# Performance work log

Hardware: AMD Instinct MI355X
Metric: run time of the kernel (lower is better)

## Reference

```python
import jax, jax.numpy as jnp
import numpy as np

N_NODES = 20000
N_EDGES = 320000
D_IN = 256      # n_source_nodes (input feature dim)
HEADS = 4
HEAD_DIM = 64   # n_target_nodes // heads
D_OUT = HEADS * HEAD_DIM  # n_target_nodes = 256
EDGE_DIM = 1


def setup_inputs() -> dict:
    key = jax.random.key(0)
    ks = jax.random.split(key, 12)
    s = 0.05
    return {
        "x": jax.random.normal(ks[0], (N_NODES, D_IN), jnp.float32),
        "edge_index": jax.random.randint(ks[1], (2, N_EDGES), 0, N_NODES, jnp.int64),
        "edge_attr": jax.random.normal(ks[2], (N_EDGES, EDGE_DIM), jnp.float32),
        # TransformerConv params (weights stored [in, out]; PyG Linear defaults: q/k/v have bias, edge lin has no bias, skip lin has bias)
        "Wq": jax.random.normal(ks[3], (D_IN, D_OUT), jnp.float32) * s,
        "bq": jnp.zeros((D_OUT,), jnp.float32),
        "Wk": jax.random.normal(ks[4], (D_IN, D_OUT), jnp.float32) * s,
        "bk": jnp.zeros((D_OUT,), jnp.float32),
        "Wv": jax.random.normal(ks[5], (D_IN, D_OUT), jnp.float32) * s,
        "bv": jnp.zeros((D_OUT,), jnp.float32),
        "We": jax.random.normal(ks[6], (EDGE_DIM, D_OUT), jnp.float32) * s,
        "Wskip": jax.random.normal(ks[7], (D_IN, D_OUT), jnp.float32) * s,
        "bskip": jnp.zeros((D_OUT,), jnp.float32),
        # GraphNorm params
        "gn_weight": jnp.ones((D_OUT,), jnp.float32),
        "gn_bias": jnp.zeros((D_OUT,), jnp.float32),
        "gn_mean_scale": jnp.ones((D_OUT,), jnp.float32),
    }


def reference(x, edge_index, edge_attr, Wq, bq, Wk, bk, Wv, bv, We, Wskip, bskip, gn_weight, gn_bias, gn_mean_scale):
    N = x.shape[0]
    src, dst = edge_index[0], edge_index[1]  # message flows src -> dst (source_to_target)

    q = (x @ Wq + bq).reshape(N, HEADS, HEAD_DIM)
    k = (x @ Wk + bk).reshape(N, HEADS, HEAD_DIM)
    v = (x @ Wv + bv).reshape(N, HEADS, HEAD_DIM)
    e = (edge_attr @ We).reshape(-1, HEADS, HEAD_DIM)  # [E, H, C]

    k_j = k[src] + e                                   # [E, H, C]
    alpha = jnp.einsum('ehc,ehc->eh', q[dst], k_j) / jnp.sqrt(jnp.float32(HEAD_DIM))

    # segment softmax over edges sharing the same target node
    a_max = jax.ops.segment_max(alpha, dst, num_segments=N)[dst]
    a_exp = jnp.exp(alpha - a_max)
    a_sum = jax.ops.segment_sum(a_exp, dst, num_segments=N)[dst]
    att = a_exp / (a_sum + 1e-16)                      # [E, H]

    msg = (v[src] + e) * att[..., None]                # [E, H, C]
    out = jax.ops.segment_sum(msg, dst, num_segments=N).reshape(N, D_OUT)
    out = out + x @ Wskip + bskip                      # root/skip connection (beta=False)

    # GraphNorm (single graph): weight*(x - alpha*mean)/sqrt(var+eps) + bias
    mean = out.mean(axis=0)
    centered = out - gn_mean_scale * mean
    var = jnp.mean(centered * centered, axis=0)
    out = gn_weight * centered * jax.lax.rsqrt(var + 1e-5) + gn_bias

    out = jax.nn.relu(out)
    xt = out.T @ out                                   # [D_OUT, D_OUT]
    xt_min, xt_max = jnp.min(xt), jnp.max(xt)
    return (xt - xt_min) / (xt_max - xt_min + 1e-8)
```

## Files before the change

### kernel.cpp

```cpp
#include <hip/hip_runtime.h>
#include <math.h>

#define N_NODES 20000
#define N_EDGES 320000
#define SK 20480

typedef short short8 __attribute__((ext_vector_type(8)));
typedef float f32x4 __attribute__((ext_vector_type(4)));

static __device__ __forceinline__ unsigned short f2bf(float f) {
    unsigned int u = __float_as_uint(f);
    u = (u + 0x7FFF + ((u >> 16) & 1)) >> 16;
    return (unsigned short)u;
}
static __device__ __forceinline__ float b2f(unsigned short u) {
    return __uint_as_float((unsigned int)u << 16);
}
static __device__ __forceinline__ float blo(unsigned int u) {
    return __uint_as_float(u << 16);
}
static __device__ __forceinline__ float bhi(unsigned int u) {
    return __uint_as_float(u & 0xFFFF0000u);
}

__global__ __launch_bounds__(256) void conv_x_k(const float* __restrict__ x,
                                                unsigned short* __restrict__ xb)
{
    const int t8 = blockIdx.x * 256 + threadIdx.x;
    const size_t base = (size_t)t8 * 8;
    if (base >= (size_t)N_NODES * 256) return;
    const float4 f0 = *(const float4*)(x + base);
    const float4 f1 = *(const float4*)(x + base + 4);
    ushort4 u0, u1;
    u0.x = f2bf(f0.x); u0.y = f2bf(f0.y); u0.z = f2bf(f0.z); u0.w = f2bf(f0.w);
    u1.x = f2bf(f1.x); u1.y = f2bf(f1.y); u1.z = f2bf(f1.z); u1.w = f2bf(f1.w);
    *(ushort4*)(xb + base) = u0;
    *(ushort4*)(xb + base + 4) = u1;
}

__global__ __launch_bounds__(256) void conv_w_k(const float* __restrict__ Wq,
                                                const float* __restrict__ Wk,
                                                const float* __restrict__ Wv,
                                                const float* __restrict__ Wsk,
                                                const float* __restrict__ bq,
                                                const float* __restrict__ bk,
                                                const float* __restrict__ bv,
                                                const float* __restrict__ bsk,
                                                unsigned short* __restrict__ wT,
                                                float* __restrict__ bias_all)
{
    const int b = blockIdx.x;
    const int kk = threadIdx.x;
    const int wi = b >> 8, n = b & 255;
    const float* W = (wi == 0) ? Wq : (wi == 1) ? Wk : (wi == 2) ? Wv : Wsk;
    wT[(size_t)b * 256 + kk] = f2bf(W[(size_t)kk * 256 + n]);
    if (kk == 0) {
        const float* bb = (wi == 0) ? bq : (wi == 1) ? bk : (wi == 2) ? bv : bsk;
        bias_all[b] = bb[n];
    }
}

__global__ __launch_bounds__(512, 2) void gemm_qkvs(const unsigned short* __restrict__ xb,
                                                    const unsigned short* __restrict__ wT,
                                                    const float* __restrict__ bias_all,
                                                    float* __restrict__ qb,
                                                    unsigned short* __restrict__ kvb,
                                                    float* __restrict__ ob)
{
    __shared__ __align__(16) unsigned short As[(128 + 256) * 80];
    unsigned short* Bs = As + 128 * 80;
    float* stage = (float*)As;

    const int tid  = threadIdx.x;
    const int lane = tid & 63;
    const int w    = tid >> 6;
    const int wm = w >> 2, wn = w & 3;
    const int row0 = blockIdx.x * 128;
    const int wsel = blockIdx.y;
    const int colG = wsel * 256;
    const int ar = tid >> 2, ak = (tid & 3) * 16;
    const int br = tid >> 1, bk = (tid & 1) * 32;
    const int fr = lane & 15, fk = (lane >> 4) * 8, lg = lane >> 4;

    f32x4 acc[4][4] = {};

    for (int k0 = 0; k0 < 256; k0 += 64) {
        int gr = row0 + ar; gr = gr < N_NODES ? gr : N_NODES - 1;
        const unsigned short* ap = xb + (size_t)gr * 256 + k0 + ak;
        const uint4 a0 = *(const uint4*)ap;
        const uint4 a1 = *(const uint4*)(ap + 8);
        const unsigned short* bp = wT + (size_t)(colG + br) * 256 + k0 + bk;
        const uint4 b0 = *(const uint4*)bp;
        const uint4 b1 = *(const uint4*)(bp + 8);
        const uint4 b2 = *(const uint4*)(bp + 16);
        const uint4 b3 = *(const uint4*)(bp + 24);
        __syncthreads();
        *(uint4*)&As[ar * 80 + ak]     = a0;
        *(uint4*)&As[ar * 80 + ak + 8] = a1;
        unsigned short* bsp = &Bs[br * 80 + bk];
        *(uint4*)bsp        = b0;
        *(uint4*)(bsp + 8)  = b1;
        *(uint4*)(bsp + 16) = b2;
        *(uint4*)(bsp + 24) = b3;
        __syncthreads();
#pragma unroll
        for (int ks = 0; ks < 2; ++ks) {
            short8 af[4], bf[4];
#pragma unroll
            for (int m = 0; m < 4; ++m)
                af[m] = *(const short8*)&As[(wm * 64 + m * 16 + fr) * 80 + ks * 32 + fk];
#pragma unroll
            for (int n = 0; n < 4; ++n)
                bf[n] = *(const short8*)&Bs[(wn * 64 + n * 16 + fr) * 80 + ks * 32 + fk];
#pragma unroll
            for (int m = 0; m < 4; ++m)
#pragma unroll
                for (int n = 0; n < 4; ++n)
                    acc[m][n] = __builtin_amdgcn_mfma_f32_16x16x32_bf16(af[m], bf[n], acc[m][n], 0, 0, 0);
        }
    }
    __syncthreads();

    float badd[4];
#pragma unroll
    for (int n = 0; n < 4; ++n) badd[n] = bias_all[colG + wn * 64 + n * 16 + fr];

    float* st = stage + w * 1024;
#pragma unroll
    for (int m = 0; m < 4; ++m) {
#pragma unroll
        for (int n = 0; n < 4; ++n)
#pragma unroll
            for (int r = 0; r < 4; ++r)
                st[(lg * 4 + r) * 64 + n * 16 + fr] = acc[m][n][r] + badd[n];
#pragma unroll
        for (int it = 0; it < 4; ++it) {
            const int lrow = it * 4 + lg;
            const f32x4 c4 = *(const f32x4*)&st[lrow * 64 + fr * 4];
            const int grow = row0 + wm * 64 + m * 16 + lrow;
            if (grow < N_NODES) {
                if (wsel == 0) {
                    float4 o; o.x = c4[0]; o.y = c4[1]; o.z = c4[2]; o.w = c4[3];
                    *(float4*)(qb + (size_t)grow * 256 + wn * 64 + fr * 4) = o;
                } else if (wsel == 3) {
                    float4 o; o.x = c4[0]; o.y = c4[1]; o.z = c4[2]; o.w = c4[3];
                    *(float4*)(ob + (size_t)grow * 256 + wn * 64 + fr * 4) = o;
                } else {
                    ushort4 u;
                    u.x = f2bf(c4[0]); u.y = f2bf(c4[1]); u.z = f2bf(c4[2]); u.w = f2bf(c4[3]);
                    const size_t kvidx = (size_t)grow * 512 + (wn * 16 + fr) * 8 + (wsel == 1 ? 0 : 4);
                    *(ushort4*)(kvb + kvidx) = u;
                }
            }
        }
    }
}

__global__ void count_deg(const int* __restrict__ dst, int* __restrict__ deg)
{
    const int e = blockIdx.x * 256 + threadIdx.x;
    if (e < N_EDGES) atomicAdd(&deg[dst[e]], 1);
}

__global__ __launch_bounds__(1024) void scan_k(const int* __restrict__ deg,
                                               int* __restrict__ row_start)
{
    __shared__ int sdeg[20480];
    const int tid = threadIdx.x;
    const int lane = tid & 63, wid = tid >> 6;
    const int CH = 20;
#pragma unroll
    for (int i = 0; i < 20; ++i) {
        const int idx = i * 1024 + tid;
        sdeg[idx] = (idx < N_NODES) ? deg[idx] : 0;
    }
    __syncthreads();
    const int base = tid * CH;
    int local[CH];
    int s = 0;
#pragma unroll
    for (int i = 0; i < CH; ++i) {
        local[i] = s;
        s += sdeg[base + i];
    }
    int v = s;
#pragma unroll
    for (int off = 1; off < 64; off <<= 1) {
        const int t = __shfl_up(v, off);
        if (lane >= off) v += t;
    }
    __shared__ int wsum[16];
    if (lane == 63) wsum[wid] = v;
    __syncthreads();
    if (tid == 0) {
        int r = 0;
        for (int i = 0; i < 16; ++i) { const int t = wsum[i]; wsum[i] = r; r += t; }
    }
    __syncthreads();
    const int excl = v - s + wsum[wid];
#pragma unroll
    for (int i = 0; i < CH; ++i) {
        const int idx = base + i;
        if (idx < N_NODES) row_start[idx] = excl + local[i];
    }
    if (tid == 1023) row_start[N_NODES] = excl + s;
}

__global__ void fill_csr(const int* __restrict__ dst, const int* __restrict__ src,
                         const float* __restrict__ ea,
                         const int* __restrict__ row_start,
                         int* __restrict__ cursor, int2* __restrict__ ekv)
{
    const int e = blockIdx.x * 256 + threadIdx.x;
    if (e < N_EDGES) {
        const int d = dst[e];
        const int p = atomicAdd(&cursor[d], 1);
        int2 pk;
        pk.x = src[e];
        pk.y = __float_as_int(ea[e]);
        ekv[row_start[d] + p] = pk;
    }
}

static __device__ __forceinline__ void edge_step(const uint4 kv, const float a,
                                                 const float4 qf, const float4 we4,
                                                 float& ssum, float& ax, float& ay,
                                                 float& az, float& aw)
{
    const float k0 = blo(kv.x), k1 = bhi(kv.x), k2 = blo(kv.y), k3 = bhi(kv.y);
    const float v0 = blo(kv.z), v1 = bhi(kv.z), v2 = blo(kv.w), v3 = bhi(kv.w);
    float p = qf.x * (k0 + a * we4.x) + qf.y * (k1 + a * we4.y)
            + qf.z * (k2 + a * we4.z) + qf.w * (k3 + a * we4.w);
    p += __shfl_xor(p, 1); p += __shfl_xor(p, 2);
    p += __shfl_xor(p, 4); p += __shfl_xor(p, 8);
    const float wgt = __expf(p * 0.125f);
    ssum += wgt;
    ax += wgt * (v0 + a * we4.x);
    ay += wgt * (v1 + a * we4.y);
    az += wgt * (v2 + a * we4.z);
    aw += wgt * (v3 + a * we4.w);
}

__global__ __launch_bounds__(256) void attn_k(const float* __restrict__ q,
                                              const unsigned short* __restrict__ kvb,
                                              const float* __restrict__ We,
                                              const int* __restrict__ row_start,
                                              const int2* __restrict__ ekv,
                                              float* __restrict__ out)
{
    const int wid  = threadIdx.x >> 6;
    const int lane = threadIdx.x & 63;
    const int n = blockIdx.x * 4 + wid;
    if (n >= N_NODES) return;

    const float4 qf  = *(const float4*)(q + (size_t)n * 256 + lane * 4);
    const float4 we4 = *(const float4*)(We + lane * 4);
    const int rs = row_start[n], re = row_start[n + 1];
    const int lo8 = lane * 8;

    float ssum = 0.f;
    float ax = 0.f, ay = 0.f, az = 0.f, aw = 0.f;

    int s = rs;
    for (; s + 4 <= re; s += 4) {
        const int2 p0 = ekv[s],     p1 = ekv[s + 1];
        const int2 p2 = ekv[s + 2], p3 = ekv[s + 3];
        const int sn0 = ((unsigned)p0.x < N_NODES) ? p0.x : 0;
        const int sn1 = ((unsigned)p1.x < N_NODES) ? p1.x : 0;
        const int sn2 = ((unsigned)p2.x < N_NODES) ? p2.x : 0;
        const int sn3 = ((unsigned)p3.x < N_NODES) ? p3.x : 0;
        const uint4 kv0 = *(const uint4*)(kvb + (size_t)sn0 * 512 + lo8);
        const uint4 kv1 = *(const uint4*)(kvb + (size_t)sn1 * 512 + lo8);
        const uint4 kv2 = *(const uint4*)(kvb + (size_t)sn2 * 512 + lo8);
        const uint4 kv3 = *(const uint4*)(kvb + (size_t)sn3 * 512 + lo8);
        edge_step(kv0, __int_as_float(p0.y), qf, we4, ssum, ax, ay, az, aw);
        edge_step(kv1, __int_as_float(p1.y), qf, we4, ssum, ax, ay, az, aw);
        edge_step(kv2, __int_as_float(p2.y), qf, we4, ssum, ax, ay, az, aw);
        edge_step(kv3, __int_as_float(p3.y), qf, we4, ssum, ax, ay, az, aw);
    }
    for (; s < re; ++s) {
        const int2 p0 = ekv[s];
        const int sn0 = ((unsigned)p0.x < N_NODES) ? p0.x : 0;
        const uint4 kv0 = *(const uint4*)(kvb + (size_t)sn0 * 512 + lo8);
        edge_step(kv0, __int_as_float(p0.y), qf, we4, ssum, ax, ay, az, aw);
    }
    const float inv = 1.f / (ssum + 1e-16f);
    const float4 sk = *(const float4*)(out + (size_t)n * 256 + lane * 4);
    float4 o;
    o.x = ax * inv + sk.x;
    o.y = ay * inv + sk.y;
    o.z = az * inv + sk.z;
    o.w = aw * inv + sk.w;
    *(float4*)(out + (size_t)n * 256 + lane * 4) = o;
}

__global__ __launch_bounds__(256) void gn_stats_k(const float* __restrict__ out,
                                                  float* __restrict__ gstats)
{
    const int c = threadIdx.x;
    float s = 0.f, s2 = 0.f;
    for (int r = blockIdx.x; r < N_NODES; r += gridDim.x) {
        const float vv = out[(size_t)r * 256 + c];
        s += vv; s2 += vv * vv;
    }
    atomicAdd(&gstats[c], s);
    atomicAdd(&gstats[256 + c], s2);
}

__global__ __launch_bounds__(256) void norm_relu_T(const float* __restrict__ ob,
                                                   const float* __restrict__ gstats,
                                                   const float* __restrict__ gw,
                                                   const float* __restrict__ gb,
                                                   const float* __restrict__ gms,
                                                   unsigned short* __restrict__ obT)
{
    __shared__ unsigned short tile[256][72];
    __shared__ float smu[256], swi[256], sbd[256];
    const int t = threadIdx.x;
    const int r0 = blockIdx.x * 64;
    {
        const float invN = 1.f / (float)N_NODES;
        const float mean = gstats[t] * invN;
        const float exx  = gstats[256 + t] * invN;
        const float mu   = gms[t] * mean;
        const float var  = exx - 2.f * mu * mean + mu * mu;
        smu[t] = mu;
        swi[t] = gw[t] * rsqrtf(var + 1e-5f);
        sbd[t] = gb[t];
    }
    __syncthreads();
    const int rr = t >> 2;
    const int row = r0 + rr;
#pragma unroll
    for (int it = 0; it < 16; ++it) {
        const int col = it * 16 + (t & 3) * 4;
        float4 f = make_float4(0.f, 0.f, 0.f, 0.f);
        if (row < N_NODES) f = *(const float4*)(ob + (size_t)row * 256 + col);
        ushort4 u;
        if (row < N_NODES) {
            u.x = f2bf(fmaxf((f.x - smu[col + 0]) * swi[col + 0] + sbd[col + 0], 0.f));
            u.y = f2bf(fmaxf((f.y - smu[col + 1]) * swi[col + 1] + sbd[col + 1], 0.f));
            u.z = f2bf(fmaxf((f.z - smu[col + 2]) * swi[col + 2] + sbd[col + 2], 0.f));
            u.w = f2bf(fmaxf((f.w - smu[col + 3]) * swi[col + 3] + sbd[col + 3], 0.f));
        } else { u.x = u.y = u.z = u.w = 0; }
        tile[col + 0][rr] = u.x;
        tile[col + 1][rr] = u.y;
        tile[col + 2][rr] = u.z;
        tile[col + 3][rr] = u.w;
    }
    __syncthreads();
#pragma unroll
    for (int it = 0; it < 8; ++it) {
        const int c = it * 32 + (t >> 3);
        const int part = t & 7;
        const uint4 x0 = *(const uint4*)&tile[c][part * 8];
        *(uint4*)(obT + (size_t)c * SK + r0 + part * 8) = x0;
    }
}

__global__ __launch_bounds__(256) void gram_k(const unsigned short* __restrict__ obT,
                                              float* __restrict__ xt)
{
    const int bi_l[10] = {0,0,0,0,1,1,1,2,2,3};
    const int bj_l[10] = {0,1,2,3,1,2,3,2,3,3};
    const int bi = bi_l[blockIdx.x], bj = bj_l[blockIdx.x];
    const int r0 = blockIdx.y * 1024;

    __shared__ __align__(16) unsigned short Ai[64 * 136];
    __shared__ __align__(16) unsigned short Aj[64 * 136];
    const int tid = threadIdx.x;
    const int lane = tid & 63;
    const int w = tid >> 6;
    const int wi = w >> 1, wj = w & 1;
    const int lr = tid >> 2, kseg = (tid & 3) * 32;
    const int fr = lane & 15, fk = (lane >> 4) * 8, lg = lane >> 4;

    f32x4 acc[2][2] = {};

    for (int kt = 0; kt < 1024; kt += 128) {
        uint4 ai[4], aj[4];
        const unsigned short* pa = obT + (size_t)(bi * 64 + lr) * SK + r0 + kt + kseg;
        const unsigned short* pb = obT + (size_t)(bj * 64 + lr) * SK + r0 + kt + kseg;
#pragma unroll
        for (int j = 0; j < 4; ++j) { ai[j] = *(const uint4*)(pa + 8 * j); aj[j] = *(const uint4*)(pb + 8 * j); }
        __syncthreads();
#pragma unroll
        for (int j = 0; j < 4; ++j) {
            *(uint4*)&Ai[lr * 136 + kseg + 8 * j] = ai[j];
            *(uint4*)&Aj[lr * 136 + kseg + 8 * j] = aj[j];
        }
        __syncthreads();
#pragma unroll
        for (int ks = 0; ks < 4; ++ks) {
            short8 af[2], bf[2];
#pragma unroll
            for (int m = 0; m < 2; ++m)
                af[m] = *(const short8*)&Ai[(wi * 32 + m * 16 + fr) * 136 + ks * 32 + fk];
#pragma unroll
            for (int n = 0; n < 2; ++n)
                bf[n] = *(const short8*)&Aj[(wj * 32 + n * 16 + fr) * 136 + ks * 32 + fk];
#pragma unroll
            for (int m = 0; m < 2; ++m)
#pragma unroll
                for (int n = 0; n < 2; ++n)
                    acc[m][n] = __builtin_amdgcn_mfma_f32_16x16x32_bf16(af[m], bf[n], acc[m][n], 0, 0, 0);
        }
    }
#pragma unroll
    for (int m = 0; m < 2; ++m)
#pragma unroll
        for (int n = 0; n < 2; ++n)
#pragma unroll
            for (int r = 0; r < 4; ++r)
                atomicAdd(&xt[(size_t)(bi * 64 + wi * 32 + m * 16 + lg * 4 + r) * 256
                              + bj * 64 + wj * 32 + n * 16 + fr], acc[m][n][r]);
}

__global__ __launch_bounds__(1024) void minmax_k(const float* __restrict__ xt,
                                                 float* __restrict__ mm)
{
    const int tid = threadIdx.x;
    float mn = 1e30f, mx = -1e30f;
    for (int i = tid; i < 65536; i += 1024) {
        const int r = i >> 8, c = i & 255;
        if ((r >> 6) <= (c >> 6)) {
            const float v = xt[i];
            mn = fminf(mn, v);
            mx = fmaxf(mx, v);
        }
    }
    for (int off = 1; off < 64; off <<= 1) {
        mn = fminf(mn, __shfl_xor(mn, off));
        mx = fmaxf(mx, __shfl_xor(mx, off));
    }
    __shared__ float smn[16], smx[16];
    const int w = tid >> 6;
    if ((tid & 63) == 0) { smn[w] = mn; smx[w] = mx; }
    __syncthreads();
    if (tid == 0) {
        for (int i = 1; i < 16; ++i) {
            mn = fminf(mn, smn[i]);
            mx = fmaxf(mx, smx[i]);
        }
        mm[0] = mn; mm[1] = mx;
    }
}

__global__ void finalize_k(const float* __restrict__ xt, const float* __restrict__ mm,
                           float* __restrict__ outp)
{
    const int i = blockIdx.x * 256 + threadIdx.x;
    const int r = i >> 8, c = i & 255;
    const float v = ((r >> 6) <= (c >> 6)) ? xt[i] : xt[c * 256 + r];
    const float mn = mm[0], mx = mm[1];
    const float inv = 1.f / (mx - mn + 1e-8f);
    outp[i] = (v - mn) * inv;
}

extern "C" void kernel_launch(void* const* d_in, const int* in_sizes, int n_in,
                              void* d_out, int out_size, void* d_ws, size_t ws_size,
                              hipStream_t stream)
{
    (void)in_sizes; (void)n_in; (void)out_size; (void)ws_size;
    const float* x   = (const float*)d_in[0];
    const int*   ei  = (const int*)d_in[1];
    const float* ea  = (const float*)d_in[2];
    const float* Wq  = (const float*)d_in[3];
    const float* bq  = (const float*)d_in[4];
    const float* Wk  = (const float*)d_in[5];
    const float* bk  = (const float*)d_in[6];
    const float* Wv  = (const float*)d_in[7];
    const float* bv  = (const float*)d_in[8];
    const float* We  = (const float*)d_in[9];
    const float* Wsk = (const float*)d_in[10];
    const float* bsk = (const float*)d_in[11];
    const float* gw  = (const float*)d_in[12];
    const float* gb  = (const float*)d_in[13];
    const float* gms = (const float*)d_in[14];
    float* outp = (float*)d_out;

    char* ws = (char*)d_ws;
    size_t off = 0;
    #define WS_ALLOC(nbytes) (ws + off); off = (off + (size_t)(nbytes) + 255) & ~(size_t)255
    unsigned short* xb  = (unsigned short*)WS_ALLOC((size_t)N_NODES * 256 * 2);
    unsigned short* wT  = (unsigned short*)WS_ALLOC((size_t)1024 * 256 * 2);
    float* bias_all     = (float*)WS_ALLOC(1024 * 4);
    float* qb           = (float*)WS_ALLOC((size_t)N_NODES * 256 * 4);
    unsigned short* kvb = (unsigned short*)WS_ALLOC((size_t)N_NODES * 512 * 2);
    float* ob           = (float*)WS_ALLOC((size_t)N_NODES * 256 * 4);
    const size_t zoff = off;
    int*   deg    = (int*)WS_ALLOC((size_t)N_NODES * 4);
    int*   cur    = (int*)WS_ALLOC((size_t)N_NODES * 4);
    float* gstats = (float*)WS_ALLOC(512 * 4);
    float* xt     = (float*)WS_ALLOC(65536 * 4);
    const size_t zbytes = off - zoff;
    int* row_start = (int*)WS_ALLOC((size_t)(N_NODES + 1) * 4);
    float* mm      = (float*)WS_ALLOC(2 * 4);
    #undef WS_ALLOC
    int2* ekv           = (int2*)xb;
    unsigned short* obT = (unsigned short*)qb;

    const int* srcv = ei;
    const int* dstv = ei + N_EDGES;

    hipMemsetAsync(ws + zoff, 0, zbytes, stream);

    conv_x_k<<<(N_NODES * 256 / 8 + 255) / 256, 256, 0, stream>>>(x, xb);
    conv_w_k<<<1024, 256, 0, stream>>>(Wq, Wk, Wv, Wsk, bq, bk, bv, bsk, wT, bias_all);

    gemm_qkvs<<<dim3((N_NODES + 127) / 128, 4), 512, 0, stream>>>(xb, wT, bias_all,
                                                                  qb, kvb, ob);

    count_deg<<<(N_EDGES + 255) / 256, 256, 0, stream>>>(dstv, deg);
    scan_k<<<1, 1024, 0, stream>>>(deg, row_start);
    fill_csr<<<(N_EDGES + 255) / 256, 256, 0, stream>>>(dstv, srcv, ea, row_start, cur, ekv);

    attn_k<<<(N_NODES + 3) / 4, 256, 0, stream>>>(qb, kvb, We, row_start, ekv, ob);

    gn_stats_k<<<400, 256, 0, stream>>>(ob, gstats);
    norm_relu_T<<<320, 256, 0, stream>>>(ob, gstats, gw, gb, gms, obT);

    gram_k<<<dim3(10, 20), 256, 0, stream>>>(obT, xt);
    minmax_k<<<1, 1024, 0, stream>>>(xt, mm);
    finalize_k<<<256, 256, 0, stream>>>(xt, mm, outp);
}
```

Baseline: 226.5 us.

## Fuse prep kernels and degree count, store q in bf16, fold GraphNorm stats into attention

Merges the x/weight bf16 conversion and the degree count into one launch. Stores q in bf16 to halve its write and read traffic, and changes the GEMM LDS row padding. Accumulates the GraphNorm column sums in the attention kernel through a per-block shared reduction and atomics, removing a separate full pass over the output. Rounding q to bf16 adds precision loss, and the block-level atomics add contention on gstats.

After: 307.6 us. 35.8% more time.

```diff
diff --git a/kernel.cpp b/kernel.cpp
--- a/kernel.cpp
+++ b/kernel.cpp
@@ -4,6 +4,7 @@
 #define N_NODES 20000
 #define N_EDGES 320000
 #define SK 20480
+#define APAD 84
 
 typedef short short8 __attribute__((ext_vector_type(8)));
 typedef float f32x4 __attribute__((ext_vector_type(4)));
@@ -23,52 +24,56 @@
     return __uint_as_float(u & 0xFFFF0000u);
 }
 
-__global__ __launch_bounds__(256) void conv_x_k(const float* __restrict__ x,
-                                                unsigned short* __restrict__ xb)
-{
-    const int t8 = blockIdx.x * 256 + threadIdx.x;
-    const size_t base = (size_t)t8 * 8;
-    if (base >= (size_t)N_NODES * 256) return;
-    const float4 f0 = *(const float4*)(x + base);
-    const float4 f1 = *(const float4*)(x + base + 4);
-    ushort4 u0, u1;
-    u0.x = f2bf(f0.x); u0.y = f2bf(f0.y); u0.z = f2bf(f0.z); u0.w = f2bf(f0.w);
-    u1.x = f2bf(f1.x); u1.y = f2bf(f1.y); u1.z = f2bf(f1.z); u1.w = f2bf(f1.w);
-    *(ushort4*)(xb + base) = u0;
-    *(ushort4*)(xb + base + 4) = u1;
-}
-
-__global__ __launch_bounds__(256) void conv_w_k(const float* __restrict__ Wq,
-                                                const float* __restrict__ Wk,
-                                                const float* __restrict__ Wv,
-                                                const float* __restrict__ Wsk,
-                                                const float* __restrict__ bq,
-                                                const float* __restrict__ bk,
-                                                const float* __restrict__ bv,
-                                                const float* __restrict__ bsk,
-                                                unsigned short* __restrict__ wT,
-                                                float* __restrict__ bias_all)
+__global__ __launch_bounds__(256) void prep_k(const float* __restrict__ x,
+                                              unsigned short* __restrict__ xb,
+                                              const float* __restrict__ Wq,
+                                              const float* __restrict__ Wk,
+                                              const float* __restrict__ Wv,
+                                              const float* __restrict__ Wsk,
+                                              const float* __restrict__ bq,
+                                              const float* __restrict__ bk,
+                                              const float* __restrict__ bv,
+                                              const float* __restrict__ bsk,
+                                              unsigned short* __restrict__ wT,
+                                              float* __restrict__ bias_all,
+                                              const int* __restrict__ dst,
+                                              int* __restrict__ deg)
 {
     const int b = blockIdx.x;
-    const int kk = threadIdx.x;
-    const int wi = b >> 8, n = b & 255;
-    const float* W = (wi == 0) ? Wq : (wi == 1) ? Wk : (wi == 2) ? Wv : Wsk;
-    wT[(size_t)b * 256 + kk] = f2bf(W[(size_t)kk * 256 + n]);
-    if (kk == 0) {
-        const float* bb = (wi == 0) ? bq : (wi == 1) ? bk : (wi == 2) ? bv : bsk;
-        bias_all[b] = bb[n];
+    const int tid = threadIdx.x;
+    if (b < 2500) {
+        const size_t base = ((size_t)b * 256 + tid) * 8;
+        const float4 f0 = *(const float4*)(x + base);
+        const float4 f1 = *(const float4*)(x + base + 4);
+        ushort4 u0, u1;
+        u0.x = f2bf(f0.x); u0.y = f2bf(f0.y); u0.z = f2bf(f0.z); u0.w = f2bf(f0.w);
+        u1.x = f2bf(f1.x); u1.y = f2bf(f1.y); u1.z = f2bf(f1.z); u1.w = f2bf(f1.w);
+        *(ushort4*)(xb + base) = u0;
+        *(ushort4*)(xb + base + 4) = u1;
+    } else if (b < 3524) {
+        const int bb = b - 2500;
+        const int wi = bb >> 8, n = bb & 255;
+        const float* W = (wi == 0) ? Wq : (wi == 1) ? Wk : (wi == 2) ? Wv : Wsk;
+        wT[(size_t)bb * 256 + tid] = f2bf(W[(size_t)tid * 256 + n]);
+        if (tid == 0) {
+            const float* bv_ = (wi == 0) ? bq : (wi == 1) ? bk : (wi == 2) ? bv : bsk;
+            bias_all[bb] = bv_[n];
+        }
+    } else {
+        const int e = (b - 3524) * 256 + tid;
+        if (e < N_EDGES) atomicAdd(&deg[dst[e]], 1);
     }
 }
 
 __global__ __launch_bounds__(512, 2) void gemm_qkvs(const unsigned short* __restrict__ xb,
                                                     const unsigned short* __restrict__ wT,
                                                     const float* __restrict__ bias_all,
-                                                    float* __restrict__ qb,
+                                                    unsigned short* __restrict__ qb,
                                                     unsigned short* __restrict__ kvb,
                                                     float* __restrict__ ob)
 {
-    __shared__ __align__(16) unsigned short As[(128 + 256) * 80];
-    unsigned short* Bs = As + 128 * 80;
+    __shared__ __align__(16) unsigned short As[(128 + 256) * APAD];
+    unsigned short* Bs = As + 128 * APAD;
     float* stage = (float*)As;
 
     const int tid  = threadIdx.x;
@@ -95,9 +100,9 @@
         const uint4 b2 = *(const uint4*)(bp + 16);
         const uint4 b3 = *(const uint4*)(bp + 24);
         __syncthreads();
-        *(uint4*)&As[ar * 80 + ak]     = a0;
-        *(uint4*)&As[ar * 80 + ak + 8] = a1;
-        unsigned short* bsp = &Bs[br * 80 + bk];
+        *(uint4*)&As[ar * APAD + ak]     = a0;
+        *(uint4*)&As[ar * APAD + ak + 8] = a1;
+        unsigned short* bsp = &Bs[br * APAD + bk];
         *(uint4*)bsp        = b0;
         *(uint4*)(bsp + 8)  = b1;
         *(uint4*)(bsp + 16) = b2;
@@ -108,10 +113,10 @@
             short8 af[4], bf[4];
 #pragma unroll
             for (int m = 0; m < 4; ++m)
-                af[m] = *(const short8*)&As[(wm * 64 + m * 16 + fr) * 80 + ks * 32 + fk];
+                af[m] = *(const short8*)&As[(wm * 64 + m * 16 + fr) * APAD + ks * 32 + fk];
 #pragma unroll
             for (int n = 0; n < 4; ++n)
-                bf[n] = *(const short8*)&Bs[(wn * 64 + n * 16 + fr) * 80 + ks * 32 + fk];
+                bf[n] = *(const short8*)&Bs[(wn * 64 + n * 16 + fr) * APAD + ks * 32 + fk];
 #pragma unroll
             for (int m = 0; m < 4; ++m)
 #pragma unroll
@@ -139,27 +144,22 @@
             const f32x4 c4 = *(const f32x4*)&st[lrow * 64 + fr * 4];
             const int grow = row0 + wm * 64 + m * 16 + lrow;
             if (grow < N_NODES) {
-                if (wsel == 0) {
-                    float4 o; o.x = c4[0]; o.y = c4[1]; o.z = c4[2]; o.w = c4[3];
-                    *(float4*)(qb + (size_t)grow * 256 + wn * 64 + fr * 4) = o;
-                } else if (wsel == 3) {
+                if (wsel == 3) {
                     float4 o; o.x = c4[0]; o.y = c4[1]; o.z = c4[2]; o.w = c4[3];
                     *(float4*)(ob + (size_t)grow * 256 + wn * 64 + fr * 4) = o;
                 } else {
                     ushort4 u;
                     u.x = f2bf(c4[0]); u.y = f2bf(c4[1]); u.z = f2bf(c4[2]); u.w = f2bf(c4[3]);
-                    const size_t kvidx = (size_t)grow * 512 + (wn * 16 + fr) * 8 + (wsel == 1 ? 0 : 4);
-                    *(ushort4*)(kvb + kvidx) = u;
+                    if (wsel == 0) {
+                        *(ushort4*)(qb + (size_t)grow * 256 + wn * 64 + fr * 4) = u;
+                    } else {
+                        const size_t kvidx = (size_t)grow * 512 + (wn * 16 + fr) * 8 + (wsel == 1 ? 0 : 4);
+                        *(ushort4*)(kvb + kvidx) = u;
+                    }
                 }
             }
         }
     }
-}
-
-__global__ void count_deg(const int* __restrict__ dst, int* __restrict__ deg)
-{
-    const int e = blockIdx.x * 256 + threadIdx.x;
-    if (e < N_EDGES) atomicAdd(&deg[dst[e]], 1);
 }
 
 __global__ __launch_bounds__(1024) void scan_k(const int* __restrict__ deg,
@@ -241,19 +241,22 @@
     aw += wgt * (v3 + a * we4.w);
 }
 
-__global__ __launch_bounds__(256) void attn_k(const float* __restrict__ q,
+__global__ __launch_bounds__(256) void attn_k(const unsigned short* __restrict__ qb,
                                               const unsigned short* __restrict__ kvb,
                                               const float* __restrict__ We,
                                               const int* __restrict__ row_start,
                                               const int2* __restrict__ ekv,
-                                              float* __restrict__ out)
-{
+                                              float* __restrict__ out,
+                                              float* __restrict__ gstats)
+{
+    __shared__ float red[4][256];
     const int wid  = threadIdx.x >> 6;
     const int lane = threadIdx.x & 63;
     const int n = blockIdx.x * 4 + wid;
-    if (n >= N_NODES) return;
-
-    const float4 qf  = *(const float4*)(q + (size_t)n * 256 + lane * 4);
+
+    const ushort4 qv = *(const ushort4*)(qb + (size_t)n * 256 + lane * 4);
+    float4 qf;
+    qf.x = b2f(qv.x); qf.y = b2f(qv.y); qf.z = b2f(qv.z); qf.w = b2f(qv.w);
     const float4 we4 = *(const float4*)(We + lane * 4);
     const int rs = row_start[n], re = row_start[n + 1];
     const int lo8 = lane * 8;
@@ -292,19 +295,18 @@
     o.z = az * inv + sk.z;
     o.w = aw * inv + sk.w;
     *(float4*)(out + (size_t)n * 256 + lane * 4) = o;
-}
-
-__global__ __launch_bounds__(256) void gn_stats_k(const float* __restrict__ out,
-                                                  float* __restrict__ gstats)
-{
+
+    *(float4*)&red[wid][lane * 4] = o;
+    __syncthreads();
     const int c = threadIdx.x;
-    float s = 0.f, s2 = 0.f;
-    for (int r = blockIdx.x; r < N_NODES; r += gridDim.x) {
-        const float vv = out[(size_t)r * 256 + c];
-        s += vv; s2 += vv * vv;
-    }
-    atomicAdd(&gstats[c], s);
-    atomicAdd(&gstats[256 + c], s2);
+    float sv = 0.f, sv2 = 0.f;
+#pragma unroll
+    for (int w2 = 0; w2 < 4; ++w2) {
+        const float v = red[w2][c];
+        sv += v; sv2 += v * v;
+    }
+    atomicAdd(&gstats[c], sv);
+    atomicAdd(&gstats[256 + c], sv2);
 }
 
 __global__ __launch_bounds__(256) void norm_relu_T(const float* __restrict__ ob,
@@ -485,7 +487,7 @@
     unsigned short* xb  = (unsigned short*)WS_ALLOC((size_t)N_NODES * 256 * 2);
     unsigned short* wT  = (unsigned short*)WS_ALLOC((size_t)1024 * 256 * 2);
     float* bias_all     = (float*)WS_ALLOC(1024 * 4);
-    float* qb           = (float*)WS_ALLOC((size_t)N_NODES * 256 * 4);
+    unsigned short* qb  = (unsigned short*)WS_ALLOC((size_t)N_NODES * 256 * 2);
     unsigned short* kvb = (unsigned short*)WS_ALLOC((size_t)N_NODES * 512 * 2);
     float* ob           = (float*)WS_ALLOC((size_t)N_NODES * 256 * 4);
     const size_t zoff = off;
@@ -498,26 +500,25 @@
     float* mm      = (float*)WS_ALLOC(2 * 4);
     #undef WS_ALLOC
     int2* ekv           = (int2*)xb;
-    unsigned short* obT = (unsigned short*)qb;
+    unsigned short* obT = (unsigned short*)xb;
 
     const int* srcv = ei;
     const int* dstv = ei + N_EDGES;
 
     hipMemsetAsync(ws + zoff, 0, zbytes, stream);
 
-    conv_x_k<<<(N_NODES * 256 / 8 + 255) / 256, 256, 0, stream>>>(x, xb);
-    conv_w_k<<<1024, 256, 0, stream>>>(Wq, Wk, Wv, Wsk, bq, bk, bv, bsk, wT, bias_all);
+    prep_k<<<2500 + 1024 + 1250, 256, 0, stream>>>(x, xb, Wq, Wk, Wv, Wsk,
+                                                   bq, bk, bv, bsk, wT, bias_all,
+                                                   dstv, deg);
 
     gemm_qkvs<<<dim3((N_NODES + 127) / 128, 4), 512, 0, stream>>>(xb, wT, bias_all,
                                                                   qb, kvb, ob);
 
-    count_deg<<<(N_EDGES + 255) / 256, 256, 0, stream>>>(dstv, deg);
     scan_k<<<1, 1024, 0, stream>>>(deg, row_start);
     fill_csr<<<(N_EDGES + 255) / 256, 256, 0, stream>>>(dstv, srcv, ea, row_start, cur, ekv);
 
-    attn_k<<<(N_NODES + 3) / 4, 256, 0, stream>>>(qb, kvb, We, row_start, ekv, ob);
-
-    gn_stats_k<<<400, 256, 0, stream>>>(ob, gstats);
+    attn_k<<<N_NODES / 4, 256, 0, stream>>>(qb, kvb, We, row_start, ekv, ob, gstats);
+
     norm_relu_T<<<320, 256, 0, stream>>>(ob, gstats, gw, gb, gms, obT);
 
     gram_k<<<dim3(10, 20), 256, 0, stream>>>(obT, xt);
```
